# Kernel tuning notes

Hardware: AMD Instinct MI355X
Metric: run time of the kernel (lower is better)

The kernel has to match this reference:

```python
import jax, jax.numpy as jnp
import numpy as np

B, LV, LT, D, TD, H = 64, 1024, 128, 256, 1536, 4
HD = D // H
KEEP_RATIO = 0.5
K = min(max(int(np.ceil(LV * KEEP_RATIO)), 1), LV)
ND = LV - K  # number of dropped tokens
EPS_NORM = 1e-12


def setup_inputs() -> dict:
    key = jax.random.key(0)
    ks = jax.random.split(key, 9)
    s = 0.02
    return {
        "hidden_v": jax.random.normal(ks[0], (B, LV, D), jnp.float32),
        "hidden_t": jax.random.normal(ks[1], (B, LT, TD), jnp.float32),
        "senti_t": jax.random.normal(ks[2], (B, LT), jnp.float32),
        "mask_v": jnp.ones((B, LV), dtype=bool),
        "mask_t": jnp.ones((B, LT), dtype=bool),
        "W_t": jax.random.normal(ks[3], (D, TD), jnp.float32) * s,
        "b_t": jnp.zeros((D,), jnp.float32),
        "Wq": jax.random.normal(ks[4], (D, D), jnp.float32) * s,
        "bq": jnp.zeros((D,), jnp.float32),
        "Wk": jax.random.normal(ks[5], (D, D), jnp.float32) * s,
        "bk": jnp.zeros((D,), jnp.float32),
    }


def _l2norm(x):
    n = jnp.linalg.norm(x, axis=-1, keepdims=True)
    return x / jnp.maximum(n, EPS_NORM)


def _prune_one(V_b, score_b):
    """V_b: [LV, D], score_b: [LV] -> (V_merge [K, D], top_idx [K])."""
    _, top_idx = jax.lax.top_k(score_b, K)
    top_idx = jnp.sort(top_idx)
    V_keep = V_b[top_idx]                       # [K, D]
    drop_mask = jnp.ones((LV,), bool).at[top_idx].set(False)
    ar = jnp.arange(LV)
    drop_idx = jnp.sort(jnp.where(drop_mask, ar, LV + ar))[:ND]  # [ND], sorted
    V_drop = V_b[drop_idx]                      # [ND, D]
    score_drop = score_b[drop_idx]              # [ND]
    # bipartite cosine-similarity assignment of dropped -> kept
    sim = _l2norm(V_drop) @ _l2norm(V_keep).T   # [ND, K]
    assign = jnp.argmax(sim, axis=1)            # [ND]
    # per-cluster softmax over dropped-token scores (segment softmax)
    seg_max = jax.ops.segment_max(score_drop, assign, num_segments=K)
    w = jnp.exp(score_drop - seg_max[assign])
    denom = jax.ops.segment_sum(w, assign, num_segments=K)
    w = w / jnp.maximum(denom[assign], EPS_NORM)
    merged = jax.ops.segment_sum(w[:, None] * V_drop, assign, num_segments=K)
    has_member = jax.ops.segment_sum(jnp.ones((ND,), V_b.dtype), assign, num_segments=K) > 0
    V_merge = _l2norm(V_keep + merged)
    V_out = jnp.where(has_member[:, None], V_merge, V_keep)
    return V_out, top_idx


def reference(hidden_v, hidden_t, senti_t, mask_v, mask_t, W_t, b_t, Wq, bq, Wk, bk):
    mt = mask_t.astype(jnp.float32)
    # text projection + sentiment weights
    T = hidden_t @ W_t.T + b_t                                   # [B, LT, D]
    w_t = jnp.abs(senti_t) * mt
    w_t = w_t / (w_t.sum(axis=1, keepdims=True) + 1e-8)
    w_t = w_t * mt
    # cross-attention weights (averaged over heads); attn_out is unused by the module
    q = (hidden_v @ Wq.T + bq).reshape(B, LV, H, HD)
    k = (T @ Wk.T + bk).reshape(B, LT, H, HD)
    scores = jnp.einsum('bqhd,bkhd->bhqk', q, k) / np.sqrt(HD)   # [B, H, LV, LT]
    scores = jnp.where(mask_t[:, None, None, :], scores, -1e9)
    attn = jax.nn.softmax(scores, axis=-1).mean(axis=1)          # [B, LV, LT]
    score_v = jnp.einsum('bqk,bk->bq', attn, w_t)                # [B, LV]
    score_v = jnp.where(mask_v, score_v, -1e9)
    hidden_v_new, retained_indices = jax.vmap(_prune_one)(hidden_v, score_v)
    return hidden_v_new, retained_indices
```

## Files before the change

kernel.cpp:

```cpp
#include <hip/hip_runtime.h>
#include <math.h>

#define B_ 64
#define LV_ 1024
#define LT_ 128
#define D_ 256
#define TD_ 1536
#define H_ 4
#define HD_ 64
#define K_ 512
#define ND_ 512

__device__ float g_M[TD_ * D_];
__device__ float g_WqT[D_ * D_];
__device__ float g_WkT[D_ * D_];
__device__ float g_kbias[D_];
__device__ float g_wt[B_ * LT_];
__device__ float g_KmatT[(size_t)B_ * D_ * LT_];
__device__ float g_score[B_ * LV_];
__device__ int   g_tidx[B_ * K_];
__device__ int   g_didx[B_ * ND_];
__device__ float g_sdrop[B_ * ND_];
__device__ int   g_assign[B_ * ND_];
__device__ float g_kninv[B_ * K_];


__device__ __forceinline__ float f4c(const float4& v, int i) {
  return ((const float*)&v)[i];
}

__global__ __launch_bounds__(256) void prep1_kernel(
    const float* __restrict__ Wk, const float* __restrict__ Wq,
    const float* __restrict__ bt, const float* __restrict__ bk) {
  int bx = blockIdx.x, t = threadIdx.x;
  if (bx < D_) {
    g_WkT[bx * D_ + t] = Wk[t * D_ + bx];
  } else if (bx < 2 * D_) {
    int j = bx - D_;
    g_WqT[j * D_ + t] = Wq[t * D_ + j];
  } else {
    float acc = bk[t];
    for (int e = 0; e < D_; ++e) acc += bt[e] * Wk[t * D_ + e];
    g_kbias[t] = acc;
  }
}

__global__ __launch_bounds__(256) void prep2_kernel(const float* __restrict__ Wt) {
  int j0 = blockIdx.x * 16;
  int t = threadIdx.x;
  __shared__ float WtL[256 * 20];
  const float4* Wt4 = (const float4*)Wt;
#pragma unroll
  for (int i = 0; i < 4; ++i) {
    int idx = i * 256 + t;
    int e = idx >> 2, j4 = idx & 3;
    float4 v = Wt4[e * (TD_ / 4) + (j0 >> 2) + j4];
    WtL[e * 20 + 4 * j4 + 0] = v.x;
    WtL[e * 20 + 4 * j4 + 1] = v.y;
    WtL[e * 20 + 4 * j4 + 2] = v.z;
    WtL[e * 20 + 4 * j4 + 3] = v.w;
  }
  __syncthreads();
  float acc[16];
#pragma unroll
  for (int jj = 0; jj < 16; ++jj) acc[jj] = 0.f;
  for (int e = 0; e < D_; ++e) {
    float wk = g_WkT[e * D_ + t];
#pragma unroll
    for (int q4 = 0; q4 < 4; ++q4) {
      float4 w = *(const float4*)&WtL[e * 20 + 4 * q4];
      acc[4 * q4 + 0] += w.x * wk;
      acc[4 * q4 + 1] += w.y * wk;
      acc[4 * q4 + 2] += w.z * wk;
      acc[4 * q4 + 3] += w.w * wk;
    }
  }
#pragma unroll
  for (int jj = 0; jj < 16; ++jj) g_M[(j0 + jj) * D_ + t] = acc[jj];
}

__global__ __launch_bounds__(128) void wt_kernel(const float* __restrict__ senti) {
  int b = blockIdx.x, t = threadIdx.x;
  __shared__ float red[128];
  float v = fabsf(senti[b * LT_ + t]);
  red[t] = v;
  __syncthreads();
  for (int s = 64; s > 0; s >>= 1) {
    if (t < s) red[t] += red[t + s];
    __syncthreads();
  }
  g_wt[b * LT_ + t] = v / (red[0] + 1e-8f);
}

__global__ __launch_bounds__(256) void kproj_kernel(const float* __restrict__ ht) {
  int b = blockIdx.x >> 3;
  int l0 = (blockIdx.x & 7) * 16;
  int t = threadIdx.x;
  __shared__ float htT[256 * 20];
  int lq = t >> 6;
  int dq = t & 63;
  float acc[4][4];
#pragma unroll
  for (int li = 0; li < 4; ++li)
#pragma unroll
    for (int di = 0; di < 4; ++di) acc[li][di] = 0.f;
  const float4* M4 = (const float4*)g_M;
  const float4* ht4 = (const float4*)ht;
  for (int e0 = 0; e0 < TD_; e0 += 256) {
    __syncthreads();
#pragma unroll
    for (int i = 0; i < 4; ++i) {
      int idx = i * 256 + t;
      int e4 = idx >> 4, l = idx & 15;
      float4 v = ht4[(size_t)(b * LT_ + l0 + l) * (TD_ / 4) + (e0 >> 2) + e4];
      htT[(4 * e4 + 0) * 20 + l] = v.x;
      htT[(4 * e4 + 1) * 20 + l] = v.y;
      htT[(4 * e4 + 2) * 20 + l] = v.z;
      htT[(4 * e4 + 3) * 20 + l] = v.w;
    }
    __syncthreads();
    for (int e = 0; e < 256; ++e) {
      float4 m = M4[(size_t)(e0 + e) * 64 + dq];
      float4 hl = *(const float4*)&htT[e * 20 + 4 * lq];
#pragma unroll
      for (int li = 0; li < 4; ++li) {
        float hs = f4c(hl, li);
        acc[li][0] += hs * m.x;
        acc[li][1] += hs * m.y;
        acc[li][2] += hs * m.z;
        acc[li][3] += hs * m.w;
      }
    }
  }
  float4 kb = *(const float4*)(g_kbias + 4 * dq);
  __syncthreads();
#pragma unroll
  for (int li = 0; li < 4; ++li) {
    float o0 = acc[li][0] + kb.x;
    float o1 = acc[li][1] + kb.y;
    float o2 = acc[li][2] + kb.z;
    float o3 = acc[li][3] + kb.w;
    int l = 4 * lq + li;
    htT[(4 * dq + 0) * 17 + l] = o0;
    htT[(4 * dq + 1) * 17 + l] = o1;
    htT[(4 * dq + 2) * 17 + l] = o2;
    htT[(4 * dq + 3) * 17 + l] = o3;
  }
  __syncthreads();
#pragma unroll
  for (int i = 0; i < 16; ++i) {
    int idx = i * 256 + t;
    int l = idx & 15, d = idx >> 4;
    g_KmatT[((size_t)b * D_ + d) * LT_ + l0 + l] = htT[d * 17 + l];
  }
}

__global__ __launch_bounds__(256, 5) void score_kernel(
    const float* __restrict__ hv, const float* __restrict__ bq) {
  int b = blockIdx.y;
  int q0 = blockIdx.x * 32;
  int t = threadIdx.x;
  __shared__ float qR[32 * 256];
  int co = t & 31;
  int rq = t >> 5;
  {
    float acc[4][8];
#pragma unroll
    for (int c = 0; c < 8; ++c) {
      float bqv = bq[8 * co + c];
#pragma unroll
      for (int ri = 0; ri < 4; ++ri) acc[ri][c] = bqv;
    }
    const float4* hv4 = (const float4*)(hv + ((size_t)b * LV_ + q0) * D_);
    for (int j4 = 0; j4 < 64; ++j4) {
      float4 hq[4];
#pragma unroll
      for (int ri = 0; ri < 4; ++ri) hq[ri] = hv4[(4 * rq + ri) * 64 + j4];
#pragma unroll
      for (int jj = 0; jj < 4; ++jj) {
        const float4* w4 = (const float4*)(g_WqT + (4 * j4 + jj) * D_ + 8 * co);
        float4 wa = w4[0], wb = w4[1];
#pragma unroll
        for (int ri = 0; ri < 4; ++ri) {
          float hvv = f4c(hq[ri], jj);
          acc[ri][0] += hvv * wa.x;
          acc[ri][1] += hvv * wa.y;
          acc[ri][2] += hvv * wa.z;
          acc[ri][3] += hvv * wa.w;
          acc[ri][4] += hvv * wb.x;
          acc[ri][5] += hvv * wb.y;
          acc[ri][6] += hvv * wb.z;
          acc[ri][7] += hvv * wb.w;
        }
      }
    }
    float4* qR4w = (float4*)qR;
#pragma unroll
    for (int ri = 0; ri < 4; ++ri) {
      qR4w[(4 * rq + ri) * 64 + 2 * co + 0] =
          make_float4(acc[ri][0], acc[ri][1], acc[ri][2], acc[ri][3]);
      qR4w[(4 * rq + ri) * 64 + 2 * co + 1] =
          make_float4(acc[ri][4], acc[ri][5], acc[ri][6], acc[ri][7]);
    }
  }
  __syncthreads();
  int qq = rq;
  int kq = co;
  float4 wtv = ((const float4*)(g_wt + b * LT_))[kq];
  float svacc[4] = {0.f, 0.f, 0.f, 0.f};
  const float4* kmt4 = (const float4*)(g_KmatT + (size_t)b * D_ * LT_);
  const float4* qR4 = (const float4*)qR;
  for (int h = 0; h < H_; ++h) {
    float sacc[4][4];
#pragma unroll
    for (int ri = 0; ri < 4; ++ri)
#pragma unroll
      for (int ki = 0; ki < 4; ++ki) sacc[ri][ki] = 0.f;
#pragma unroll
    for (int d4 = 0; d4 < 16; ++d4) {
      float4 qv[4], kv[4];
#pragma unroll
      for (int ri = 0; ri < 4; ++ri)
        qv[ri] = qR4[(4 * qq + ri) * 64 + h * 16 + d4];
#pragma unroll
      for (int dd = 0; dd < 4; ++dd)
        kv[dd] = kmt4[(size_t)(h * 64 + 4 * d4 + dd) * 32 + kq];
#pragma unroll
      for (int dd = 0; dd < 4; ++dd)
#pragma unroll
        for (int ri = 0; ri < 4; ++ri) {
          float qs = f4c(qv[ri], dd);
          sacc[ri][0] += qs * kv[dd].x;
          sacc[ri][1] += qs * kv[dd].y;
          sacc[ri][2] += qs * kv[dd].z;
          sacc[ri][3] += qs * kv[dd].w;
        }
    }
#pragma unroll
    for (int ri = 0; ri < 4; ++ri) {
      float s0 = sacc[ri][0] * 0.125f, s1 = sacc[ri][1] * 0.125f;
      float s2 = sacc[ri][2] * 0.125f, s3 = sacc[ri][3] * 0.125f;
      float m = fmaxf(fmaxf(s0, s1), fmaxf(s2, s3));
#pragma unroll
      for (int off = 16; off > 0; off >>= 1) m = fmaxf(m, __shfl_xor(m, off));
      float e0 = expf(s0 - m), e1 = expf(s1 - m);
      float e2 = expf(s2 - m), e3 = expf(s3 - m);
      float es = e0 + e1 + e2 + e3;
      float cs = e0 * wtv.x + e1 * wtv.y + e2 * wtv.z + e3 * wtv.w;
#pragma unroll
      for (int off = 16; off > 0; off >>= 1) {
        es += __shfl_xor(es, off);
        cs += __shfl_xor(cs, off);
      }
      svacc[ri] += cs / es;
    }
  }
  if (kq == 0) {
#pragma unroll
    for (int ri = 0; ri < 4; ++ri)
      g_score[(size_t)b * LV_ + q0 + 4 * qq + ri] = svacc[ri] * 0.25f;
  }
}

__global__ __launch_bounds__(1024) void topk_kernel(float* __restrict__ out_idx) {
  int b = blockIdx.x, t = threadIdx.x;
  __shared__ float s[LV_];
  __shared__ unsigned char keep[LV_];
  s[t] = g_score[(size_t)b * LV_ + t];
  __syncthreads();
  float mys = s[t];
  int cnt = 0;
  for (int jj = 0; jj < LV_; ++jj) {
    float sj = s[jj];
    cnt += (sj > mys || (sj == mys && jj < t)) ? 1 : 0;
  }
  int kp = (cnt < K_) ? 1 : 0;
  keep[t] = (unsigned char)kp;
  __syncthreads();
  int pos = 0;
  for (int jj = 0; jj < t; ++jj) pos += keep[jj];
  if (kp) {
    g_tidx[b * K_ + pos] = t;
    out_idx[b * K_ + pos] = (float)t;
  } else {
    int dp = t - pos;
    g_didx[b * ND_ + dp] = t;
    g_sdrop[b * ND_ + dp] = mys;
  }
}

__global__ __launch_bounds__(256) void knorm_kernel(const float* __restrict__ hv) {
  int b = blockIdx.y;
  int k = blockIdx.x * 256 + threadIdx.x;
  int src = g_tidx[b * K_ + k];
  const float4* row = (const float4*)(hv + ((size_t)b * LV_ + src) * D_);
  float acc = 0.f;
  for (int c = 0; c < 64; ++c) {
    float4 v = row[c];
    acc += v.x * v.x;
    acc += v.y * v.y;
    acc += v.z * v.z;
    acc += v.w * v.w;
  }
  g_kninv[b * K_ + k] = 1.f / fmaxf(sqrtf(acc), 1e-12f);
}

__global__ __launch_bounds__(256, 3) void assign_kernel(const float* __restrict__ hv) {
  int b = blockIdx.y;
  int n0 = blockIdx.x * 32;
  int t = threadIdx.x;
  __shared__ float smem[32 * 9 * 4 + 32 * 128];
  float* VdL = smem;
  float* VkT = smem + 1152;
  float* bestv = smem;
  int* bestk = (int*)(smem + 1024);

  int tn = t >> 5;
  int tk = t & 31;
  int rstage = t >> 3;
  int c8 = t & 7;

  int didx_t = g_didx[b * ND_ + n0 + rstage];
  const float4* vd_src = (const float4*)(hv + ((size_t)b * LV_ + didx_t) * D_);

  float bv[4] = {-INFINITY, -INFINITY, -INFINITY, -INFINITY};
  int bk[4] = {0, 0, 0, 0};

  for (int kt = 0; kt < 4; ++kt) {
    const float4* vk_src[4];
#pragma unroll
    for (int i = 0; i < 4; ++i) {
      int kl = i * 32 + rstage;
      int tix = g_tidx[b * K_ + kt * 128 + kl];
      vk_src[i] = (const float4*)(hv + ((size_t)b * LV_ + tix) * D_);
    }
    float4 kn4 = ((const float4*)(g_kninv + (size_t)b * K_ + kt * 128))[tk];
    float acc[4][4][4];
#pragma unroll
    for (int ri = 0; ri < 4; ++ri)
#pragma unroll
      for (int kj = 0; kj < 4; ++kj)
#pragma unroll
        for (int c = 0; c < 4; ++c) acc[ri][kj][c] = 0.f;
    for (int dc = 0; dc < 8; ++dc) {
      __syncthreads();
      {
        float4 v = vd_src[dc * 8 + c8];
        ((float4*)VdL)[rstage * 9 + c8] = v;
      }
#pragma unroll
      for (int i = 0; i < 4; ++i) {
        int kl = i * 32 + rstage;
        float4 v = vk_src[i][dc * 8 + c8];
        int col = ((((kl >> 2) ^ c8) << 2) | (kl & 3));
        VkT[(4 * c8 + 0) * 128 + col] = v.x;
        VkT[(4 * c8 + 1) * 128 + col] = v.y;
        VkT[(4 * c8 + 2) * 128 + col] = v.z;
        VkT[(4 * c8 + 3) * 128 + col] = v.w;
      }
      __syncthreads();
      const float4* VdL4 = (const float4*)VdL;
      const float4* VkT4 = (const float4*)VkT;
#pragma unroll
      for (int d4l = 0; d4l < 8; ++d4l) {
        float4 vd[4], kv[4];
#pragma unroll
        for (int ri = 0; ri < 4; ++ri)
          vd[ri] = VdL4[(4 * tn + ri) * 9 + d4l];
#pragma unroll
        for (int dd = 0; dd < 4; ++dd)
          kv[dd] = VkT4[(4 * d4l + dd) * 32 + (tk ^ d4l)];
#pragma unroll
        for (int dd = 0; dd < 4; ++dd)
#pragma unroll
          for (int ri = 0; ri < 4; ++ri) {
            float a = f4c(vd[ri], dd);
            acc[ri][0][dd] += a * kv[dd].x;
            acc[ri][1][dd] += a * kv[dd].y;
            acc[ri][2][dd] += a * kv[dd].z;
            acc[ri][3][dd] += a * kv[dd].w;
          }
      }
    }
#pragma unroll
    for (int ri = 0; ri < 4; ++ri) {
#pragma unroll
      for (int kj = 0; kj < 4; ++kj) {
        float s = (acc[ri][kj][0] + acc[ri][kj][1]) + (acc[ri][kj][2] + acc[ri][kj][3]);
        float v = s * f4c(kn4, kj);
        int kg = kt * 128 + 4 * tk + kj;
        if (v > bv[ri]) { bv[ri] = v; bk[ri] = kg; }
      }
    }
  }
  __syncthreads();
#pragma unroll
  for (int ri = 0; ri < 4; ++ri) {
    bestv[(4 * tn + ri) * 32 + tk] = bv[ri];
    bestk[(4 * tn + ri) * 32 + tk] = bk[ri];
  }
  __syncthreads();
  if (t < 32) {
    float bvf = bestv[t * 32];
    int bkf = bestk[t * 32];
    for (int q = 1; q < 32; ++q) {
      float v = bestv[t * 32 + q];
      int kx = bestk[t * 32 + q];
      if (v > bvf || (v == bvf && kx < bkf)) { bvf = v; bkf = kx; }
    }
    g_assign[b * ND_ + n0 + t] = bkf;
  }
}

__global__ __launch_bounds__(64) void merge_kernel(
    const float* __restrict__ hv, float* __restrict__ out_v) {
  int b = blockIdx.y, k = blockIdx.x;
  int lane = threadIdx.x;
  __shared__ int mem[ND_];
  int base = 0;
  for (int c = 0; c < ND_; c += 64) {
    int a = g_assign[b * ND_ + c + lane];
    unsigned long long msk = __ballot(a == k);
    if (a == k) {
      int pos = base + __popcll(msk & ((1ULL << lane) - 1ULL));
      mem[pos] = c + lane;
    }
    base += __popcll(msk);
  }
  __syncthreads();
  int src = g_tidx[b * K_ + k];
  float4 vk = ((const float4*)(hv + ((size_t)b * LV_ + src) * D_))[lane];
  float4 res;
  if (base > 0) {
    float mx = -INFINITY;
    for (int i = lane; i < base; i += 64) mx = fmaxf(mx, g_sdrop[b * ND_ + mem[i]]);
#pragma unroll
    for (int o = 32; o > 0; o >>= 1) mx = fmaxf(mx, __shfl_xor(mx, o));
    float dsum = 0.f;
    for (int i = lane; i < base; i += 64) dsum += expf(g_sdrop[b * ND_ + mem[i]] - mx);
#pragma unroll
    for (int o = 32; o > 0; o >>= 1) dsum += __shfl_xor(dsum, o);
    dsum = fmaxf(dsum, 1e-12f);
    float4 acc = {0.f, 0.f, 0.f, 0.f};
    for (int i = 0; i < base; ++i) {
      int n = mem[i];
      float w = expf(g_sdrop[b * ND_ + n] - mx) / dsum;
      float4 ud = ((const float4*)(hv + ((size_t)b * LV_ + g_didx[b * ND_ + n]) * D_))[lane];
      acc.x += w * ud.x; acc.y += w * ud.y;
      acc.z += w * ud.z; acc.w += w * ud.w;
    }
    float4 s4 = {vk.x + acc.x, vk.y + acc.y, vk.z + acc.z, vk.w + acc.w};
    float ss = s4.x * s4.x + s4.y * s4.y + s4.z * s4.z + s4.w * s4.w;
#pragma unroll
    for (int o = 32; o > 0; o >>= 1) ss += __shfl_xor(ss, o);
    float scale = 1.f / fmaxf(sqrtf(ss), 1e-12f);
    res.x = s4.x * scale; res.y = s4.y * scale; res.z = s4.z * scale; res.w = s4.w * scale;
  } else {
    res = vk;
  }
  ((float4*)(out_v + ((size_t)b * K_ + k) * D_))[lane] = res;
}

extern "C" void kernel_launch(void* const* d_in, const int* in_sizes, int n_in,
                              void* d_out, int out_size, void* d_ws, size_t ws_size,
                              hipStream_t stream) {
  const float* hv = (const float*)d_in[0];
  const float* ht = (const float*)d_in[1];
  const float* senti = (const float*)d_in[2];
  const float* Wt = (const float*)d_in[5];
  const float* bt = (const float*)d_in[6];
  const float* Wq = (const float*)d_in[7];
  const float* bq = (const float*)d_in[8];
  const float* Wk = (const float*)d_in[9];
  const float* bk = (const float*)d_in[10];
  (void)in_sizes; (void)n_in; (void)out_size; (void)d_ws; (void)ws_size;

  float* out_v = (float*)d_out;
  float* out_idx = out_v + (size_t)B_ * K_ * D_;

  hipLaunchKernelGGL(prep1_kernel, dim3(2 * D_ + 1), dim3(256), 0, stream, Wk, Wq, bt, bk);
  hipLaunchKernelGGL(prep2_kernel, dim3(TD_ / 16), dim3(256), 0, stream, Wt);
  hipLaunchKernelGGL(wt_kernel, dim3(B_), dim3(128), 0, stream, senti);
  hipLaunchKernelGGL(kproj_kernel, dim3(B_ * 8), dim3(256), 0, stream, ht);
  hipLaunchKernelGGL(score_kernel, dim3(LV_ / 32, B_), dim3(256), 0, stream, hv, bq);
  hipLaunchKernelGGL(topk_kernel, dim3(B_), dim3(1024), 0, stream, out_idx);
  hipLaunchKernelGGL(knorm_kernel, dim3(2, B_), dim3(256), 0, stream, hv);
  hipLaunchKernelGGL(assign_kernel, dim3(ND_ / 32, B_), dim3(256), 0, stream, hv);
  hipLaunchKernelGGL(merge_kernel, dim3(K_, B_), dim3(64), 0, stream, hv, out_v);
}
```

Before: 834.3 us.

## Split Q projection from score kernel and stage K tiles in shared memory

The fused score kernel is split in two. One kernel computes the Q projection and writes it to a global buffer. A second kernel reads Q from global memory and stages K^T chunks in LDS, prefetching the next chunk into registers while computing on the current one. The goal is to cut the fused kernel's large shared-memory footprint and its repeated global K loads, at the cost of writing and re-reading a 64 MB Q buffer plus one extra launch.

```diff
diff --git a/kernel.cpp b/kernel.cpp
--- a/kernel.cpp
+++ b/kernel.cpp
@@ -17,6 +17,7 @@
 __device__ float g_kbias[D_];
 __device__ float g_wt[B_ * LT_];
 __device__ float g_KmatT[(size_t)B_ * D_ * LT_];
+__device__ float g_Q[(size_t)B_ * LV_ * D_];
 __device__ float g_score[B_ * LV_];
 __device__ int   g_tidx[B_ * K_];
 __device__ int   g_didx[B_ * ND_];
@@ -155,86 +156,112 @@
   }
 }
 
-__global__ __launch_bounds__(256, 5) void score_kernel(
+__global__ __launch_bounds__(256) void qproj_kernel(
     const float* __restrict__ hv, const float* __restrict__ bq) {
   int b = blockIdx.y;
   int q0 = blockIdx.x * 32;
   int t = threadIdx.x;
-  __shared__ float qR[32 * 256];
   int co = t & 31;
   int rq = t >> 5;
-  {
-    float acc[4][8];
-#pragma unroll
-    for (int c = 0; c < 8; ++c) {
-      float bqv = bq[8 * co + c];
-#pragma unroll
-      for (int ri = 0; ri < 4; ++ri) acc[ri][c] = bqv;
-    }
-    const float4* hv4 = (const float4*)(hv + ((size_t)b * LV_ + q0) * D_);
-    for (int j4 = 0; j4 < 64; ++j4) {
-      float4 hq[4];
-#pragma unroll
-      for (int ri = 0; ri < 4; ++ri) hq[ri] = hv4[(4 * rq + ri) * 64 + j4];
-#pragma unroll
-      for (int jj = 0; jj < 4; ++jj) {
-        const float4* w4 = (const float4*)(g_WqT + (4 * j4 + jj) * D_ + 8 * co);
-        float4 wa = w4[0], wb = w4[1];
-#pragma unroll
-        for (int ri = 0; ri < 4; ++ri) {
-          float hvv = f4c(hq[ri], jj);
-          acc[ri][0] += hvv * wa.x;
-          acc[ri][1] += hvv * wa.y;
-          acc[ri][2] += hvv * wa.z;
-          acc[ri][3] += hvv * wa.w;
-          acc[ri][4] += hvv * wb.x;
-          acc[ri][5] += hvv * wb.y;
-          acc[ri][6] += hvv * wb.z;
-          acc[ri][7] += hvv * wb.w;
-        }
-      }
-    }
-    float4* qR4w = (float4*)qR;
-#pragma unroll
-    for (int ri = 0; ri < 4; ++ri) {
-      qR4w[(4 * rq + ri) * 64 + 2 * co + 0] =
-          make_float4(acc[ri][0], acc[ri][1], acc[ri][2], acc[ri][3]);
-      qR4w[(4 * rq + ri) * 64 + 2 * co + 1] =
-          make_float4(acc[ri][4], acc[ri][5], acc[ri][6], acc[ri][7]);
-    }
-  }
-  __syncthreads();
-  int qq = rq;
-  int kq = co;
+  float acc[4][8];
+#pragma unroll
+  for (int c = 0; c < 8; ++c) {
+    float bqv = bq[8 * co + c];
+#pragma unroll
+    for (int ri = 0; ri < 4; ++ri) acc[ri][c] = bqv;
+  }
+  const float4* hv4 = (const float4*)(hv + ((size_t)b * LV_ + q0) * D_);
+  for (int j4 = 0; j4 < 64; ++j4) {
+    float4 hq[4];
+#pragma unroll
+    for (int ri = 0; ri < 4; ++ri) hq[ri] = hv4[(4 * rq + ri) * 64 + j4];
+#pragma unroll
+    for (int jj = 0; jj < 4; ++jj) {
+      const float4* w4 = (const float4*)(g_WqT + (4 * j4 + jj) * D_ + 8 * co);
+      float4 wa = w4[0], wb = w4[1];
+#pragma unroll
+      for (int ri = 0; ri < 4; ++ri) {
+        float hvv = f4c(hq[ri], jj);
+        acc[ri][0] += hvv * wa.x;
+        acc[ri][1] += hvv * wa.y;
+        acc[ri][2] += hvv * wa.z;
+        acc[ri][3] += hvv * wa.w;
+        acc[ri][4] += hvv * wb.x;
+        acc[ri][5] += hvv * wb.y;
+        acc[ri][6] += hvv * wb.z;
+        acc[ri][7] += hvv * wb.w;
+      }
+    }
+  }
+  float4* gQ4 = (float4*)(g_Q + ((size_t)b * LV_ + q0) * D_);
+#pragma unroll
+  for (int ri = 0; ri < 4; ++ri) {
+    gQ4[(4 * rq + ri) * 64 + 2 * co + 0] =
+        make_float4(acc[ri][0], acc[ri][1], acc[ri][2], acc[ri][3]);
+    gQ4[(4 * rq + ri) * 64 + 2 * co + 1] =
+        make_float4(acc[ri][4], acc[ri][5], acc[ri][6], acc[ri][7]);
+  }
+}
+
+__global__ __launch_bounds__(256) void score2_kernel() {
+  int b = blockIdx.y;
+  int q0 = blockIdx.x * 32;
+  int t = threadIdx.x;
+  __shared__ float kT[32 * 128];
+  int kq = t & 31;
+  int qq = t >> 5;
   float4 wtv = ((const float4*)(g_wt + b * LT_))[kq];
   float svacc[4] = {0.f, 0.f, 0.f, 0.f};
   const float4* kmt4 = (const float4*)(g_KmatT + (size_t)b * D_ * LT_);
-  const float4* qR4 = (const float4*)qR;
+  const float4* gQ4 = (const float4*)(g_Q + ((size_t)b * LV_ + q0) * D_);
+  float4* kT4w = (float4*)kT;
+  const float4* kT4 = (const float4*)kT;
+  float4 pre[4];
+#pragma unroll
+  for (int i = 0; i < 4; ++i) {
+    int idx = i * 256 + t;
+    pre[i] = kmt4[(idx >> 5) * 32 + (idx & 31)];
+  }
   for (int h = 0; h < H_; ++h) {
     float sacc[4][4];
 #pragma unroll
     for (int ri = 0; ri < 4; ++ri)
 #pragma unroll
       for (int ki = 0; ki < 4; ++ki) sacc[ri][ki] = 0.f;
-#pragma unroll
-    for (int d4 = 0; d4 < 16; ++d4) {
-      float4 qv[4], kv[4];
-#pragma unroll
-      for (int ri = 0; ri < 4; ++ri)
-        qv[ri] = qR4[(4 * qq + ri) * 64 + h * 16 + d4];
-#pragma unroll
-      for (int dd = 0; dd < 4; ++dd)
-        kv[dd] = kmt4[(size_t)(h * 64 + 4 * d4 + dd) * 32 + kq];
-#pragma unroll
-      for (int dd = 0; dd < 4; ++dd)
-#pragma unroll
-        for (int ri = 0; ri < 4; ++ri) {
-          float qs = f4c(qv[ri], dd);
-          sacc[ri][0] += qs * kv[dd].x;
-          sacc[ri][1] += qs * kv[dd].y;
-          sacc[ri][2] += qs * kv[dd].z;
-          sacc[ri][3] += qs * kv[dd].w;
+    for (int half = 0; half < 2; ++half) {
+      if (h | half) __syncthreads();
+#pragma unroll
+      for (int i = 0; i < 4; ++i) kT4w[i * 256 + t] = pre[i];
+      int s = h * 2 + half + 1;
+      if (s < 8) {
+        int hn = s >> 1, hf = s & 1;
+#pragma unroll
+        for (int i = 0; i < 4; ++i) {
+          int idx = i * 256 + t;
+          pre[i] = kmt4[(size_t)(hn * 64 + hf * 32 + (idx >> 5)) * 32 + (idx & 31)];
         }
+      }
+      __syncthreads();
+#pragma unroll
+      for (int d4l = 0; d4l < 8; ++d4l) {
+        float4 qv[4], kv[4];
+#pragma unroll
+        for (int ri = 0; ri < 4; ++ri)
+          qv[ri] = gQ4[(4 * qq + ri) * 64 + h * 16 + half * 8 + d4l];
+#pragma unroll
+        for (int dd = 0; dd < 4; ++dd)
+          kv[dd] = kT4[(4 * d4l + dd) * 32 + kq];
+#pragma unroll
+        for (int dd = 0; dd < 4; ++dd)
+#pragma unroll
+          for (int ri = 0; ri < 4; ++ri) {
+            float qs = f4c(qv[ri], dd);
+            sacc[ri][0] += qs * kv[dd].x;
+            sacc[ri][1] += qs * kv[dd].y;
+            sacc[ri][2] += qs * kv[dd].z;
+            sacc[ri][3] += qs * kv[dd].w;
+          }
+      }
     }
 #pragma unroll
     for (int ri = 0; ri < 4; ++ri) {
@@ -482,7 +509,8 @@
   hipLaunchKernelGGL(prep2_kernel, dim3(TD_ / 16), dim3(256), 0, stream, Wt);
   hipLaunchKernelGGL(wt_kernel, dim3(B_), dim3(128), 0, stream, senti);
   hipLaunchKernelGGL(kproj_kernel, dim3(B_ * 8), dim3(256), 0, stream, ht);
-  hipLaunchKernelGGL(score_kernel, dim3(LV_ / 32, B_), dim3(256), 0, stream, hv, bq);
+  hipLaunchKernelGGL(qproj_kernel, dim3(LV_ / 32, B_), dim3(256), 0, stream, hv, bq);
+  hipLaunchKernelGGL(score2_kernel, dim3(LV_ / 32, B_), dim3(256), 0, stream);
   hipLaunchKernelGGL(topk_kernel, dim3(B_), dim3(1024), 0, stream, out_idx);
   hipLaunchKernelGGL(knorm_kernel, dim3(2, B_), dim3(256), 0, stream, hv);
   hipLaunchKernelGGL(assign_kernel, dim3(ND_ / 32, B_), dim3(256), 0, stream, hv);
```

After: 902.1 us. 8.1% more time.
